# Optimization experiments

Hardware: AMD Instinct MI355X
Metric: run time of the kernel (lower is better)

The kernel has to match this reference:

```python
import jax, jax.numpy as jnp
import numpy as np

D_MODEL = 768
N_HEADS = 12
D_HEAD = 64
BATCH = 4
SEQ = 2048
INIT_RANGE = 0.02
IGNORE = -1e5


def setup_inputs() -> dict:
    key = jax.random.key(0)
    ks = jax.random.split(key, 5)
    x = jax.random.normal(ks[0], (BATCH, SEQ, D_MODEL), dtype=jnp.float32)
    W_Q = jax.random.normal(ks[1], (N_HEADS, D_MODEL, D_HEAD), dtype=jnp.float32) * INIT_RANGE
    W_K = jax.random.normal(ks[2], (N_HEADS, D_MODEL, D_HEAD), dtype=jnp.float32) * INIT_RANGE
    W_V = jax.random.normal(ks[3], (N_HEADS, D_MODEL, D_HEAD), dtype=jnp.float32) * INIT_RANGE
    W_O = jax.random.normal(ks[4], (N_HEADS, D_HEAD, D_MODEL), dtype=jnp.float32) * INIT_RANGE
    b_Q = jnp.zeros((N_HEADS, D_HEAD), dtype=jnp.float32)
    b_K = jnp.zeros((N_HEADS, D_HEAD), dtype=jnp.float32)
    b_V = jnp.zeros((N_HEADS, D_HEAD), dtype=jnp.float32)
    b_O = jnp.zeros((D_MODEL,), dtype=jnp.float32)
    return {"normalized_resid_pre": x, "W_Q": W_Q, "W_K": W_K, "W_V": W_V,
            "W_O": W_O, "b_Q": b_Q, "b_K": b_K, "b_V": b_V, "b_O": b_O}


def reference(normalized_resid_pre, W_Q, W_K, W_V, W_O, b_Q, b_K, b_V, b_O):
    x = normalized_resid_pre  # [b, s, d_model]
    q = jnp.einsum('bsm,hmd->bshd', x, W_Q) + b_Q  # [b, s, h, d_head]
    k = jnp.einsum('bsm,hmd->bshd', x, W_K) + b_K
    v = jnp.einsum('bsm,hmd->bshd', x, W_V) + b_V
    scores = jnp.einsum('bqhd,bkhd->bhqk', q, k) / jnp.sqrt(jnp.float32(D_HEAD))
    seq = x.shape[1]
    causal = jnp.tril(jnp.ones((seq, seq), dtype=bool))  # True where allowed
    scores = jnp.where(causal, scores, jnp.float32(IGNORE))
    pattern = jax.nn.softmax(scores, axis=-1)  # [b, h, q, k]
    z = jnp.einsum('bhqk,bkhd->bqhd', pattern, v)
    attn_out = jnp.einsum('bqhd,hdm->bqm', z, W_O) + b_O
    return attn_out
```

## Files before the change

### kernel.cpp

```cpp
#include <hip/hip_runtime.h>
#include <math.h>

#define DEVI __device__ __forceinline__

typedef __bf16 bf16_t;
typedef bf16_t bf16x8 __attribute__((ext_vector_type(8)));
typedef float  f32x4  __attribute__((ext_vector_type(4)));

constexpr int NB   = 4;
constexpr int SEQL = 2048;
constexpr int NH   = 12;
constexpr int DHD  = 64;
constexpr int DMOD = 768;
constexpr int NT   = NB * SEQL;
constexpr int KD   = DMOD;


DEVI unsigned short f2bf(float f) {
  union { float f; unsigned u; } v; v.f = f;
  unsigned r = v.u + 0x7FFFu + ((v.u >> 16) & 1u);
  return (unsigned short)(r >> 16);
}

DEVI unsigned short cvt_bf16(float f) {
  bf16_t b = (bf16_t)f;
  return __builtin_bit_cast(unsigned short, b);
}

DEVI float exp2_raw(float x) {
  float r;
  asm("v_exp_f32 %0, %1" : "=v"(r) : "v"(x));
  return r;
}

DEVI void gload16(const unsigned short* src, unsigned short* dst) {
  auto g = (const __attribute__((address_space(1))) unsigned int*)(unsigned long long)src;
  auto l = (__attribute__((address_space(3))) unsigned int*)(unsigned int)(unsigned long long)(dst);
  __builtin_amdgcn_global_load_lds(g, l, 16, 0, 0);
}

__global__ void __launch_bounds__(256) prep_all(const float* __restrict__ x,
                                                const float* __restrict__ WQ,
                                                const float* __restrict__ WK,
                                                const float* __restrict__ WV,
                                                const float* __restrict__ WO,
                                                unsigned short* __restrict__ xb,
                                                unsigned short* __restrict__ Wt,
                                                unsigned short* __restrict__ Wo_t) {
  __shared__ float T[64][68];
  const int bid = blockIdx.x;
  const int t = threadIdx.x;
  if (bid < 3072) {
    size_t i = ((size_t)bid * 256 + t) * 8;
    float4 a = *(const float4*)(x + i);
    float4 b = *(const float4*)(x + i + 4);
    union { unsigned short u[8]; uint4 v; } pk;
    pk.u[0] = f2bf(a.x); pk.u[1] = f2bf(a.y); pk.u[2] = f2bf(a.z); pk.u[3] = f2bf(a.w);
    pk.u[4] = f2bf(b.x); pk.u[5] = f2bf(b.y); pk.u[6] = f2bf(b.z); pk.u[7] = f2bf(b.w);
    *(uint4*)(xb + i) = pk.v;
    return;
  }
  const int r0 = t >> 4, c4 = (t & 15) * 4;
  if (bid < 3504) {
    const int u = bid - 3072;
    const int mt = u % 12, hw = u / 12;
    const int which = hw / 12, h = hw % 12;
    const float* W = (which == 0) ? WQ : ((which == 1) ? WK : WV);
    const float* src = W + ((size_t)h * 768 + mt * 64) * 64;
#pragma unroll
    for (int rep = 0; rep < 4; ++rep) {
      int m = rep * 16 + r0;
      float4 v = *(const float4*)(src + m * 64 + c4);
      T[m][c4] = v.x; T[m][c4 + 1] = v.y; T[m][c4 + 2] = v.z; T[m][c4 + 3] = v.w;
    }
    __syncthreads();
    unsigned short* dst = Wt + ((size_t)which * 768 + h * 64) * 768 + mt * 64;
#pragma unroll
    for (int rep = 0; rep < 4; ++rep) {
      int d = rep * 16 + r0;
      union { unsigned short u[4]; uint2 v; } o;
#pragma unroll
      for (int j = 0; j < 4; ++j) o.u[j] = f2bf(T[c4 + j][d]);
      *(uint2*)(dst + (size_t)d * 768 + c4) = o.v;
    }
  } else {
    const int u = bid - 3504;
    const int m0 = (u % 12) * 64, hd0 = (u / 12) * 64;
#pragma unroll
    for (int rep = 0; rep < 4; ++rep) {
      int i = rep * 16 + r0;
      float4 v = *(const float4*)(WO + (size_t)(hd0 + i) * 768 + m0 + c4);
      T[i][c4] = v.x; T[i][c4 + 1] = v.y; T[i][c4 + 2] = v.z; T[i][c4 + 3] = v.w;
    }
    __syncthreads();
#pragma unroll
    for (int rep = 0; rep < 4; ++rep) {
      int m = rep * 16 + r0;
      union { unsigned short u[4]; uint2 v; } o;
#pragma unroll
      for (int j = 0; j < 4; ++j) o.u[j] = f2bf(T[c4 + j][m]);
      *(uint2*)(Wo_t + (size_t)(m0 + m) * 768 + hd0 + c4) = o.v;
    }
  }
}

__global__ void __launch_bounds__(256)
gemm_qkv(const unsigned short* __restrict__ A,
         const unsigned short* __restrict__ Bt,
         const float* __restrict__ bq, const float* __restrict__ bk,
         const float* __restrict__ bv,
         unsigned short* __restrict__ qo, unsigned short* __restrict__ ko,
         unsigned short* __restrict__ vo) {
  __shared__ __align__(16) unsigned short ldsA[2 * 8192];
  __shared__ __align__(16) unsigned short ldsB[8192];
  const int bm = blockIdx.x, bn = blockIdx.y;
  const int m0 = bm * 128, n0 = bn * 128;
  const int tid = threadIdx.x, w = tid >> 6, lane = tid & 63;
  const int g = lane >> 4, r16 = lane & 15;
  const int wm = w >> 1, wn = w & 1;

  const int ss = (lane & 7) ^ ((lane >> 3) & 7);
  const unsigned short* asrc = A  + (size_t)(m0 + (lane >> 3)) * KD + ss * 8;
  const unsigned short* bsrc = Bt + (size_t)(n0 + (lane >> 3)) * KD + ss * 8;

  auto stageA = [&](int buf, int kt) {
#pragma unroll
    for (int j = 0; j < 4; ++j) {
      int seg = w * 4 + j;
      gload16(asrc + (size_t)(seg * 8) * KD + kt * 64, ldsA + buf * 8192 + seg * 512);
    }
  };
  auto stageB = [&](int kt) {
#pragma unroll
    for (int j = 0; j < 4; ++j) {
      int seg = w * 4 + j;
      gload16(bsrc + (size_t)(seg * 8) * KD + kt * 64, ldsB + seg * 512);
    }
  };

  const int r7 = r16 & 7;
  const int aoff0 = r16 * 64 + ((g    ) ^ r7) * 8;
  const int aoff1 = r16 * 64 + ((g + 4) ^ r7) * 8;

  f32x4 acc[4][4];
  const f32x4 zero4 = {0.f, 0.f, 0.f, 0.f};
#pragma unroll
  for (int i = 0; i < 4; ++i)
#pragma unroll
    for (int j = 0; j < 4; ++j) acc[i][j] = zero4;

  constexpr int NKT = KD / 64;
  stageA(0, 0);
  stageB(0);
  int buf = 0;
  for (int kt = 0; kt < NKT; ++kt) {
    if (kt + 1 < NKT) {
      stageA(buf ^ 1, kt + 1);
      asm volatile("s_waitcnt vmcnt(4)" ::: "memory");
    } else {
      asm volatile("s_waitcnt vmcnt(0)" ::: "memory");
    }
    __builtin_amdgcn_s_barrier();
    const unsigned short* Ab = ldsA + buf * 8192 + wm * 4096;
    const unsigned short* Bb = ldsB + wn * 4096;
    bf16x8 af[2][4], bfr[2][4];
#pragma unroll
    for (int f = 0; f < 4; ++f) {
      af[0][f]  = *(const bf16x8*)&Ab[aoff0 + f * 1024];
      af[1][f]  = *(const bf16x8*)&Ab[aoff1 + f * 1024];
      bfr[0][f] = *(const bf16x8*)&Bb[aoff0 + f * 1024];
      bfr[1][f] = *(const bf16x8*)&Bb[aoff1 + f * 1024];
    }
#pragma unroll
    for (int kk = 0; kk < 2; ++kk)
#pragma unroll
      for (int fm = 0; fm < 4; ++fm)
#pragma unroll
        for (int fn = 0; fn < 4; ++fn)
          acc[fm][fn] = __builtin_amdgcn_mfma_f32_16x16x32_bf16(af[kk][fm], bfr[kk][fn],
                                                                acc[fm][fn], 0, 0, 0);
    asm volatile("s_waitcnt lgkmcnt(0)" ::: "memory");
    __builtin_amdgcn_s_barrier();
    if (kt + 1 < NKT) stageB(kt + 1);
    buf ^= 1;
  }

#pragma unroll
  for (int fm = 0; fm < 4; ++fm) {
#pragma unroll
    for (int fn = 0; fn < 4; ++fn) {
      const int col = n0 + wn * 64 + fn * 16 + r16;
      const int rbase = m0 + wm * 64 + fm * 16 + g * 4;
      const int which = (col >= 1536) ? 2 : ((col >= 768) ? 1 : 0);
      const int hd = col - which * 768;
      const int h = hd >> 6, d = hd & 63;
      const float bias = (which == 0 ? bq : which == 1 ? bk : bv)[hd];
      if (which == 2) {
        union { unsigned short u[4]; uint2 v; } o;
#pragma unroll
        for (int r = 0; r < 4; ++r) o.u[r] = cvt_bf16(acc[fm][fn][r] + bias);
        const int b = rbase >> 11, s = rbase & (SEQL - 1);
        *(uint2*)(vo + ((size_t)(b * NH + h) * DHD + d) * SEQL + s) = o.v;
      } else {
#pragma unroll
        for (int r = 0; r < 4; ++r) {
          int row = rbase + r;
          int b = row >> 11, s = row & (SEQL - 1);
          float v = acc[fm][fn][r] + bias;
          if (which == 0)
            qo[((size_t)(b * NH + h) * SEQL + s) * DHD + d] = cvt_bf16(v * 0.1803368801111f);
          else
            ko[((size_t)(b * NH + h) * SEQL + s) * DHD + d] = cvt_bf16(v);
        }
      }
    }
  }
}

__global__ void __launch_bounds__(256)
gemm_o(const unsigned short* __restrict__ A,
       const unsigned short* __restrict__ Bt,
       const float* __restrict__ bo, float* __restrict__ fout) {
  __shared__ __align__(16) unsigned short ldsA[2 * 4096];
  __shared__ __align__(16) unsigned short ldsB[8192];
  const int bm = blockIdx.x, bn = blockIdx.y;
  const int m0 = bm * 64, n0 = bn * 128;
  const int tid = threadIdx.x, w = tid >> 6, lane = tid & 63;
  const int g = lane >> 4, r16 = lane & 15;
  const int wm = w >> 1, wn = w & 1;

  const int ss = (lane & 7) ^ ((lane >> 3) & 7);
  const unsigned short* asrc = A  + (size_t)(m0 + (lane >> 3)) * KD + ss * 8;
  const unsigned short* bsrc = Bt + (size_t)(n0 + (lane >> 3)) * KD + ss * 8;

  auto stageA = [&](int buf, int kt) {
#pragma unroll
    for (int j = 0; j < 2; ++j) {
      int seg = w * 2 + j;
      gload16(asrc + (size_t)(seg * 8) * KD + kt * 64, ldsA + buf * 4096 + seg * 512);
    }
  };
  auto stageB = [&](int kt) {
#pragma unroll
    for (int j = 0; j < 4; ++j) {
      int seg = w * 4 + j;
      gload16(bsrc + (size_t)(seg * 8) * KD + kt * 64, ldsB + seg * 512);
    }
  };

  const int r7 = r16 & 7;
  const int aoff0 = r16 * 64 + ((g    ) ^ r7) * 8;
  const int aoff1 = r16 * 64 + ((g + 4) ^ r7) * 8;

  f32x4 acc[2][4];
  const f32x4 zero4 = {0.f, 0.f, 0.f, 0.f};
#pragma unroll
  for (int i = 0; i < 2; ++i)
#pragma unroll
    for (int j = 0; j < 4; ++j) acc[i][j] = zero4;

  constexpr int NKT = KD / 64;
  stageA(0, 0);
  stageB(0);
  int buf = 0;
  for (int kt = 0; kt < NKT; ++kt) {
    if (kt + 1 < NKT) {
      stageA(buf ^ 1, kt + 1);
      asm volatile("s_waitcnt vmcnt(2)" ::: "memory");
    } else {
      asm volatile("s_waitcnt vmcnt(0)" ::: "memory");
    }
    __builtin_amdgcn_s_barrier();
    const unsigned short* Ab = ldsA + buf * 4096 + wm * 2048;
    const unsigned short* Bb = ldsB + wn * 4096;
    bf16x8 af[2][2], bfr[2][4];
#pragma unroll
    for (int f = 0; f < 2; ++f) {
      af[0][f] = *(const bf16x8*)&Ab[aoff0 + f * 1024];
      af[1][f] = *(const bf16x8*)&Ab[aoff1 + f * 1024];
    }
#pragma unroll
    for (int f = 0; f < 4; ++f) {
      bfr[0][f] = *(const bf16x8*)&Bb[aoff0 + f * 1024];
      bfr[1][f] = *(const bf16x8*)&Bb[aoff1 + f * 1024];
    }
#pragma unroll
    for (int kk = 0; kk < 2; ++kk)
#pragma unroll
      for (int fm = 0; fm < 2; ++fm)
#pragma unroll
        for (int fn = 0; fn < 4; ++fn)
          acc[fm][fn] = __builtin_amdgcn_mfma_f32_16x16x32_bf16(af[kk][fm], bfr[kk][fn],
                                                                acc[fm][fn], 0, 0, 0);
    asm volatile("s_waitcnt lgkmcnt(0)" ::: "memory");
    __builtin_amdgcn_s_barrier();
    if (kt + 1 < NKT) stageB(kt + 1);
    buf ^= 1;
  }

#pragma unroll
  for (int fm = 0; fm < 2; ++fm) {
#pragma unroll
    for (int fn = 0; fn < 4; ++fn) {
      const int col = n0 + wn * 64 + fn * 16 + r16;
      const int rbase = m0 + wm * 32 + fm * 16 + g * 4;
      const float bias = bo[col];
#pragma unroll
      for (int r = 0; r < 4; ++r)
        fout[(size_t)(rbase + r) * DMOD + col] = acc[fm][fn][r] + bias;
    }
  }
}

__global__ void __launch_bounds__(256, 3)
attn_fwd(const unsigned short* __restrict__ qb,
         const unsigned short* __restrict__ kb,
         const unsigned short* __restrict__ vt,
         unsigned short* __restrict__ zb) {
  __shared__ __align__(16) unsigned short ldsK[2 * 4096];
  __shared__ __align__(16) unsigned short ldsV[2 * 4096];
  __shared__ __align__(16) unsigned short ldsP[2 * 4096];
  const int id = blockIdx.x;
  const int qp = id / 48, bh = id % 48;
  const int qtA = qp, qtB = 31 - qp;
  const int tid = threadIdx.x, w = tid >> 6, lane = tid & 63;
  const int g = lane >> 4, r16 = lane & 15;
  const int r7 = r16 & 7;

  const int sslot = (lane & 7) ^ (lane >> 3);
  const unsigned short* ksrc = kb + (size_t)bh * SEQL * DHD + (lane >> 3) * 64 + sslot * 8;
  const unsigned short* vsrc = vt + (size_t)bh * SEQL * DHD + (lane >> 3) * 2048 + sslot * 8;

  auto stage = [&](int buf, int kv0) {
#pragma unroll
    for (int j = 0; j < 2; ++j) {
      int seg = w * 2 + j;
      gload16(ksrc + kv0 * 64 + seg * 512, ldsK + buf * 4096 + seg * 512);
      gload16(vsrc + kv0 + seg * 16384,    ldsV + buf * 4096 + seg * 512);
    }
  };

  const int roff0 = r16 * 64 + ((g    ) ^ r7) * 8;
  const int roff1 = r16 * 64 + ((g + 4) ^ r7) * 8;
  char* const pwbA = (char*)ldsP + w * 2048;
  char* const pwbB = (char*)ldsP + 8192 + w * 2048;
  int paddr[4];
#pragma unroll
  for (int fn = 0; fn < 4; ++fn)
    paddr[fn] = r16 * 128 + ((((fn * 2) + (g >> 1)) ^ r7) << 4) + ((g & 1) << 3);
  const int prd0 = r16 * 128 + (((g    ) ^ r7) << 4);
  const int prd1 = r16 * 128 + (((g + 4) ^ r7) << 4);
  const int thr = w * 16 + r16 - g * 4;

  bf16x8 qfA[2], qfB[2];
  {
    const unsigned short* qa = qb + ((size_t)bh * SEQL + qtA * 64 + w * 16 + r16) * DHD + g * 8;
    const unsigned short* qc = qb + ((size_t)bh * SEQL + qtB * 64 + w * 16 + r16) * DHD + g * 8;
    qfA[0] = *(const bf16x8*)qa; qfA[1] = *(const bf16x8*)(qa + 32);
    qfB[0] = *(const bf16x8*)qc; qfB[1] = *(const bf16x8*)(qc + 32);
  }

  float laccA = 0.f, laccB = 0.f;
  f32x4 zaccA[4], zaccB[4], saccA[4], saccB[4];
  const f32x4 zero4 = {0.f, 0.f, 0.f, 0.f};
#pragma unroll
  for (int r = 0; r < 4; ++r) { zaccA[r] = zero4; zaccB[r] = zero4; }

  auto qk = [&](const bf16x8* qf, f32x4* sacc, int buf) {
    const unsigned short* Kb = ldsK + buf * 4096;
    __builtin_amdgcn_s_setprio(1);
#pragma unroll
    for (int fn = 0; fn < 4; ++fn) {
      bf16x8 kf = *(const bf16x8*)&Kb[roff0 + fn * 1024];
      sacc[fn] = __builtin_amdgcn_mfma_f32_16x16x32_bf16(kf, qf[0], zero4, 0, 0, 0);
    }
#pragma unroll
    for (int fn = 0; fn < 4; ++fn) {
      bf16x8 kf = *(const bf16x8*)&Kb[roff1 + fn * 1024];
      sacc[fn] = __builtin_amdgcn_mfma_f32_16x16x32_bf16(kf, qf[1], sacc[fn], 0, 0, 0);
    }
    __builtin_amdgcn_s_setprio(0);
  };

  auto sm = [&](f32x4* sacc, float& lacc, char* pwb, bool diag) {
    if (diag) {
#pragma unroll
      for (int fn = 0; fn < 4; ++fn)
#pragma unroll
        for (int r = 0; r < 4; ++r)
          if (fn * 16 + r > thr) sacc[fn][r] = -3.0e38f;
    }
#pragma unroll
    for (int fn = 0; fn < 4; ++fn) {
      float p0 = exp2_raw(sacc[fn][0]), p1 = exp2_raw(sacc[fn][1]);
      float p2 = exp2_raw(sacc[fn][2]), p3 = exp2_raw(sacc[fn][3]);
      lacc += (p0 + p1) + (p2 + p3);
      unsigned w0, w1;
      asm("v_cvt_pk_bf16_f32 %0, %1, %2" : "=v"(w0) : "v"(p0), "v"(p1));
      asm("v_cvt_pk_bf16_f32 %0, %1, %2" : "=v"(w1) : "v"(p2), "v"(p3));
      uint2 pk; pk.x = w0; pk.y = w1;
      *(uint2*)(pwb + paddr[fn]) = pk;
    }
  };

  auto pv = [&](char* pwb, f32x4* zacc, int buf) {
    const unsigned short* Vb = ldsV + buf * 4096;
    bf16x8 pf0 = *(const bf16x8*)(pwb + prd0);
    bf16x8 pf1 = *(const bf16x8*)(pwb + prd1);
    __builtin_amdgcn_s_setprio(1);
#pragma unroll
    for (int fn = 0; fn < 4; ++fn) {
      bf16x8 vf = *(const bf16x8*)&Vb[roff0 + fn * 1024];
      zacc[fn] = __builtin_amdgcn_mfma_f32_16x16x32_bf16(pf0, vf, zacc[fn], 0, 0, 0);
    }
#pragma unroll
    for (int fn = 0; fn < 4; ++fn) {
      bf16x8 vf = *(const bf16x8*)&Vb[roff1 + fn * 1024];
      zacc[fn] = __builtin_amdgcn_mfma_f32_16x16x32_bf16(pf1, vf, zacc[fn], 0, 0, 0);
    }
    __builtin_amdgcn_s_setprio(0);
  };

  stage(0, 0);
  asm volatile("s_waitcnt vmcnt(0)" ::: "memory");
  __builtin_amdgcn_s_barrier();

  int buf = 0;
  for (int kt = 0; kt <= qtB; ++kt) {
    if (kt) __builtin_amdgcn_s_barrier();
    if (kt < qtB) {
      stage(buf ^ 1, (kt + 1) * 64);
      if (kt) asm volatile("s_waitcnt vmcnt(4)" ::: "memory");
    } else {
      asm volatile("s_waitcnt vmcnt(0)" ::: "memory");
    }
    const bool doA = (kt <= qtA);
    qk(qfB, saccB, buf);
    if (doA) qk(qfA, saccA, buf);
    sm(saccB, laccB, pwbB, kt == qtB);
    if (doA) sm(saccA, laccA, pwbA, kt == qtA);
    asm volatile("" ::: "memory");
    pv(pwbB, zaccB, buf);
    if (doA) pv(pwbA, zaccA, buf);
    buf ^= 1;
  }

  laccA += __shfl_xor(laccA, 16); laccA += __shfl_xor(laccA, 32);
  laccB += __shfl_xor(laccB, 16); laccB += __shfl_xor(laccB, 32);
  const float invA = 1.0f / laccA;
  const float invB = 1.0f / laccB;
  const int b = bh / NH, h = bh % NH;
#pragma unroll
  for (int r = 0; r < 4; ++r) {
    float iar = __shfl(invA, g * 4 + r);
    float ibr = __shfl(invB, g * 4 + r);
    int sA = qtA * 64 + w * 16 + g * 4 + r;
    int sB = qtB * 64 + w * 16 + g * 4 + r;
#pragma unroll
    for (int fn = 0; fn < 4; ++fn) {
      int d = fn * 16 + r16;
      zb[((size_t)(b * SEQL + sA)) * DMOD + h * DHD + d] = cvt_bf16(zaccA[fn][r] * iar);
      zb[((size_t)(b * SEQL + sB)) * DMOD + h * DHD + d] = cvt_bf16(zaccB[fn][r] * ibr);
    }
  }
}


extern "C" void kernel_launch(void* const* d_in, const int* in_sizes, int n_in,
                              void* d_out, int out_size, void* d_ws, size_t ws_size,
                              hipStream_t stream) {
  const float* x  = (const float*)d_in[0];
  const float* WQ = (const float*)d_in[1];
  const float* WK = (const float*)d_in[2];
  const float* WV = (const float*)d_in[3];
  const float* WO = (const float*)d_in[4];
  const float* bQ = (const float*)d_in[5];
  const float* bK = (const float*)d_in[6];
  const float* bV = (const float*)d_in[7];
  const float* bO = (const float*)d_in[8];
  float* out = (float*)d_out;

  constexpr size_t NE = (size_t)NT * DMOD;
  unsigned short* w0   = (unsigned short*)d_ws;
  unsigned short* Wqkv = w0;
  unsigned short* Wo   = Wqkv + (size_t)3 * 768 * 768;
  unsigned short* xb   = Wo + (size_t)768 * 768;
  unsigned short* qb   = xb + NE;
  unsigned short* kb   = qb + NE;
  unsigned short* vt   = kb + NE;
  unsigned short* zb   = xb;
  size_t need = (size_t)(vt + NE - w0) * sizeof(unsigned short);
  if (ws_size < need) return;

  prep_all<<<3648, 256, 0, stream>>>(x, WQ, WK, WV, WO, xb, Wqkv, Wo);
  gemm_qkv<<<dim3(64, 18), 256, 0, stream>>>(xb, Wqkv, bQ, bK, bV, qb, kb, vt);
  attn_fwd<<<768, 256, 0, stream>>>(qb, kb, vt, zb);
  gemm_o<<<dim3(128, 6), 256, 0, stream>>>(zb, Wo, bO, out);
}
```

Baseline: 106.0 us.

## Load K fragments directly from global into registers, bypassing LDS

```diff
diff --git a/kernel.cpp b/kernel.cpp
--- a/kernel.cpp
+++ b/kernel.cpp
@@ -317,7 +317,6 @@
          const unsigned short* __restrict__ kb,
          const unsigned short* __restrict__ vt,
          unsigned short* __restrict__ zb) {
-  __shared__ __align__(16) unsigned short ldsK[2 * 4096];
   __shared__ __align__(16) unsigned short ldsV[2 * 4096];
   __shared__ __align__(16) unsigned short ldsP[2 * 4096];
   const int id = blockIdx.x;
@@ -328,15 +327,22 @@
   const int r7 = r16 & 7;
 
   const int sslot = (lane & 7) ^ (lane >> 3);
-  const unsigned short* ksrc = kb + (size_t)bh * SEQL * DHD + (lane >> 3) * 64 + sslot * 8;
   const unsigned short* vsrc = vt + (size_t)bh * SEQL * DHD + (lane >> 3) * 2048 + sslot * 8;
-
-  auto stage = [&](int buf, int kv0) {
+  const unsigned short* kfsrc = kb + (size_t)bh * SEQL * DHD + r16 * 64 + g * 8;
+
+  auto stageV = [&](int buf, int kv0) {
 #pragma unroll
     for (int j = 0; j < 2; ++j) {
       int seg = w * 2 + j;
-      gload16(ksrc + kv0 * 64 + seg * 512, ldsK + buf * 4096 + seg * 512);
-      gload16(vsrc + kv0 + seg * 16384,    ldsV + buf * 4096 + seg * 512);
+      gload16(vsrc + kv0 + seg * 16384, ldsV + buf * 4096 + seg * 512);
+    }
+  };
+  auto loadK = [&](bf16x8* kr, int kv0) {
+    const unsigned short* p = kfsrc + (size_t)kv0 * 64;
+#pragma unroll
+    for (int fn = 0; fn < 4; ++fn) {
+      kr[fn]     = *(const bf16x8*)(p + fn * 1024);
+      kr[4 + fn] = *(const bf16x8*)(p + fn * 1024 + 32);
     }
   };
 
@@ -365,22 +371,6 @@
   const f32x4 zero4 = {0.f, 0.f, 0.f, 0.f};
 #pragma unroll
   for (int r = 0; r < 4; ++r) { zaccA[r] = zero4; zaccB[r] = zero4; }
-
-  auto qk = [&](const bf16x8* qf, f32x4* sacc, int buf) {
-    const unsigned short* Kb = ldsK + buf * 4096;
-    __builtin_amdgcn_s_setprio(1);
-#pragma unroll
-    for (int fn = 0; fn < 4; ++fn) {
-      bf16x8 kf = *(const bf16x8*)&Kb[roff0 + fn * 1024];
-      sacc[fn] = __builtin_amdgcn_mfma_f32_16x16x32_bf16(kf, qf[0], zero4, 0, 0, 0);
-    }
-#pragma unroll
-    for (int fn = 0; fn < 4; ++fn) {
-      bf16x8 kf = *(const bf16x8*)&Kb[roff1 + fn * 1024];
-      sacc[fn] = __builtin_amdgcn_mfma_f32_16x16x32_bf16(kf, qf[1], sacc[fn], 0, 0, 0);
-    }
-    __builtin_amdgcn_s_setprio(0);
-  };
 
   auto sm = [&](f32x4* sacc, float& lacc, char* pwb, bool diag) {
     if (diag) {
@@ -403,11 +393,9 @@
     }
   };
 
-  auto pv = [&](char* pwb, f32x4* zacc, int buf) {
-    const unsigned short* Vb = ldsV + buf * 4096;
+  auto pv = [&](char* pwb, f32x4* zacc, const unsigned short* Vb) {
     bf16x8 pf0 = *(const bf16x8*)(pwb + prd0);
     bf16x8 pf1 = *(const bf16x8*)(pwb + prd1);
-    __builtin_amdgcn_s_setprio(1);
 #pragma unroll
     for (int fn = 0; fn < 4; ++fn) {
       bf16x8 vf = *(const bf16x8*)&Vb[roff0 + fn * 1024];
@@ -418,31 +406,49 @@
       bf16x8 vf = *(const bf16x8*)&Vb[roff1 + fn * 1024];
       zacc[fn] = __builtin_amdgcn_mfma_f32_16x16x32_bf16(pf1, vf, zacc[fn], 0, 0, 0);
     }
-    __builtin_amdgcn_s_setprio(0);
-  };
-
-  stage(0, 0);
+  };
+
+  bf16x8 kcur[8], knxt[8];
+
+  stageV(0, 0);
+  loadK(kcur, 0);
   asm volatile("s_waitcnt vmcnt(0)" ::: "memory");
   __builtin_amdgcn_s_barrier();
 
-  int buf = 0;
   for (int kt = 0; kt <= qtB; ++kt) {
     if (kt) __builtin_amdgcn_s_barrier();
     if (kt < qtB) {
-      stage(buf ^ 1, (kt + 1) * 64);
-      if (kt) asm volatile("s_waitcnt vmcnt(4)" ::: "memory");
+      stageV((kt + 1) & 1, (kt + 1) * 64);
+      loadK(knxt, (kt + 1) * 64);
+      if (kt) asm volatile("s_waitcnt vmcnt(10)" ::: "memory");
     } else {
       asm volatile("s_waitcnt vmcnt(0)" ::: "memory");
     }
     const bool doA = (kt <= qtA);
-    qk(qfB, saccB, buf);
-    if (doA) qk(qfA, saccA, buf);
+    const unsigned short* Vb = ldsV + (kt & 1) * 4096;
+    __builtin_amdgcn_s_setprio(1);
+#pragma unroll
+    for (int fn = 0; fn < 4; ++fn) {
+      saccB[fn] = __builtin_amdgcn_mfma_f32_16x16x32_bf16(kcur[fn], qfB[0], zero4, 0, 0, 0);
+      if (doA) saccA[fn] = __builtin_amdgcn_mfma_f32_16x16x32_bf16(kcur[fn], qfA[0], zero4, 0, 0, 0);
+    }
+#pragma unroll
+    for (int fn = 0; fn < 4; ++fn) {
+      saccB[fn] = __builtin_amdgcn_mfma_f32_16x16x32_bf16(kcur[4 + fn], qfB[1], saccB[fn], 0, 0, 0);
+      if (doA) saccA[fn] = __builtin_amdgcn_mfma_f32_16x16x32_bf16(kcur[4 + fn], qfA[1], saccA[fn], 0, 0, 0);
+    }
+    __builtin_amdgcn_s_setprio(0);
     sm(saccB, laccB, pwbB, kt == qtB);
     if (doA) sm(saccA, laccA, pwbA, kt == qtA);
     asm volatile("" ::: "memory");
-    pv(pwbB, zaccB, buf);
-    if (doA) pv(pwbA, zaccA, buf);
-    buf ^= 1;
+    __builtin_amdgcn_s_setprio(1);
+    pv(pwbB, zaccB, Vb);
+    if (doA) pv(pwbA, zaccA, Vb);
+    __builtin_amdgcn_s_setprio(0);
+    if (kt < qtB) {
+#pragma unroll
+      for (int i = 0; i < 8; ++i) kcur[i] = knxt[i];
+    }
   }
 
   laccA += __shfl_xor(laccA, 16); laccA += __shfl_xor(laccA, 32);
```

After: 310.1 us. 192% more time.
